# Kernel tuning notes

Hardware: AMD Instinct MI355X
Metric: run time of the kernel (lower is better)

Reference implementation:

```python
import jax, jax.numpy as jnp
import numpy as np

H = 768      # hidden_size
NH = 12      # num_heads
HD = H // NH # head_size
MLP = 3072
B, N = 16, 577


def setup_inputs() -> dict:
    key = jax.random.key(0)
    ks = jax.random.split(key, 16)
    s = 0.02
    return {
        "x": jax.random.normal(ks[0], (B, N, H), jnp.float32),
        "Wq": jax.random.normal(ks[1], (H, H), jnp.float32) * s,
        "bq": jnp.zeros((H,), jnp.float32),
        "Wk": jax.random.normal(ks[2], (H, H), jnp.float32) * s,
        "bk": jnp.zeros((H,), jnp.float32),
        "Wv": jax.random.normal(ks[3], (H, H), jnp.float32) * s,
        "bv": jnp.zeros((H,), jnp.float32),
        "Wo": jax.random.normal(ks[4], (H, H), jnp.float32) * s,
        "bo": jnp.zeros((H,), jnp.float32),
        "W1": jax.random.normal(ks[5], (H, MLP), jnp.float32) * s,
        "b1": jnp.zeros((MLP,), jnp.float32),
        "W2": jax.random.normal(ks[6], (MLP, H), jnp.float32) * s,
        "b2": jnp.zeros((H,), jnp.float32),
        "ln1_g": jnp.ones((H,), jnp.float32),
        "ln1_b": jnp.zeros((H,), jnp.float32),
        "ln2_g": jnp.ones((H,), jnp.float32),
        "ln2_b": jnp.zeros((H,), jnp.float32),
    }


def _layernorm(x, g, b, eps=1e-6):
    mu = jnp.mean(x, axis=-1, keepdims=True)
    var = jnp.mean(jnp.square(x - mu), axis=-1, keepdims=True)
    return (x - mu) * jax.lax.rsqrt(var + eps) * g + b


def reference(x, Wq, bq, Wk, bk, Wv, bv, Wo, bo, W1, b1, W2, b2,
              ln1_g, ln1_b, ln2_g, ln2_b):
    h = x
    y = _layernorm(x, ln1_g, ln1_b)
    # projections [B,N,H] -> [B,NH,N,HD]
    def heads(t):
        return t.reshape(B, N, NH, HD).transpose(0, 2, 1, 3)
    q = heads(y @ Wq + bq)
    _k = heads(y @ Wk + bk)  # computed but UNUSED (bug in original: Q@V^T)
    v = heads(y @ Wv + bv)
    # faithful to source: scores = Q @ V^T (not K)
    scores = jnp.einsum('bhqd,bhkd->bhqk', q, v) / jnp.sqrt(jnp.float32(HD))
    probs = jax.nn.softmax(scores, axis=-1)
    o = jnp.einsum('bhqk,bhkd->bhqd', probs, v)
    o = o.transpose(0, 2, 1, 3).reshape(B, N, H)
    attn_out = o @ Wo + bo
    x1 = attn_out + h
    h2 = x1
    y2 = _layernorm(x1, ln2_g, ln2_b)
    m = jax.nn.gelu(y2 @ W1 + b1, approximate=False)
    m = m @ W2 + b2
    return m + h2
```

## Files before the change

### kernel.cpp

```cpp
#include <hip/hip_runtime.h>


#define GLOBAL_AS __attribute__((address_space(1)))
#define LDS_AS __attribute__((address_space(3)))

typedef __bf16 bf16x8 __attribute__((ext_vector_type(8)));
typedef float f32x4 __attribute__((ext_vector_type(4)));
typedef unsigned short u16x8 __attribute__((ext_vector_type(8)));

static __device__ __forceinline__ f32x4 mfma16(bf16x8 a, bf16x8 b, f32x4 c) {
  return __builtin_amdgcn_mfma_f32_16x16x32_bf16(a, b, c, 0, 0, 0);
}

static __device__ __forceinline__ unsigned short f2bf(float f) {
  union { float f; unsigned u; } v; v.f = f;
  unsigned r = v.u + 0x7fffu + ((v.u >> 16) & 1u);
  return (unsigned short)(r >> 16);
}

static __device__ __forceinline__ void async16(const void* g, void* l) {
  __builtin_amdgcn_global_load_lds((const GLOBAL_AS void*)g, (LDS_AS void*)l, 16, 0, 0);
}

static __device__ __forceinline__ float gelu_exact(float x) {
  return 0.5f * x * (1.0f + erff(x * 0.70710678118654752f));
}

static __device__ __forceinline__ void tc_body(const float* __restrict__ W,
                                               unsigned short* __restrict__ Wt,
                                               int K, int ldw, int nb, int kb,
                                               int t) {
  __shared__ float tile[32][33];
  const int tr = t >> 5, tc = t & 31;
#pragma unroll
  for (int p = 0; p < 4; ++p)
    tile[p * 8 + tr][tc] = W[(size_t)(kb + p * 8 + tr) * ldw + nb + tc];
  __syncthreads();
#pragma unroll
  for (int p = 0; p < 4; ++p)
    Wt[(size_t)(nb + p * 8 + tr) * K + kb + tc] = f2bf(tile[tc][p * 8 + tr]);
}

__global__ __launch_bounds__(256)
void transpose_all(const float* __restrict__ Wq, const float* __restrict__ Wv,
                   const float* __restrict__ Wo, const float* __restrict__ W1,
                   const float* __restrict__ W2, unsigned short* __restrict__ R3) {
  const size_t S = 589824;
  int id = blockIdx.x;
  const int t = threadIdx.x;
  if (id < 1728) {
    const float* W = id < 576 ? Wq : (id < 1152 ? Wv : Wo);
    unsigned short* dst = R3 + (size_t)(id / 576) * S;
    id %= 576;
    tc_body(W, dst, 768, 768, (id % 24) * 32, (id / 24) * 32, t);
  } else {
    id -= 1728;
    const int seg = id / 1152;
    id %= 1152;
    const int s = seg >> 1;
    if ((seg & 1) == 0) {
      unsigned short* dst = R3 + 3 * S + (size_t)s * 4 * S;
      tc_body(W1 + s * 1536, dst, 768, 3072, (id % 48) * 32, (id / 48) * 32, t);
    } else {
      unsigned short* dst = R3 + 5 * S + (size_t)s * 4 * S;
      tc_body(W2 + (size_t)s * 1536 * 768, dst, 1536, 768, (id % 24) * 32,
              (id / 24) * 32, t);
    }
  }
}

__global__ __launch_bounds__(256)
void ln_f32(const float* __restrict__ x, const float* __restrict__ g,
            const float* __restrict__ be, unsigned short* __restrict__ y) {
  const int w = threadIdx.x >> 6, lane = threadIdx.x & 63;
  const size_t row = (size_t)blockIdx.x * 4 + w;
  const float* xr = x + row * 768;
  float vv[12];
#pragma unroll
  for (int j = 0; j < 3; ++j) {
    float4 v = *(const float4*)(xr + j * 256 + lane * 4);
    vv[j * 4 + 0] = v.x; vv[j * 4 + 1] = v.y;
    vv[j * 4 + 2] = v.z; vv[j * 4 + 3] = v.w;
  }
  float s = 0.f;
#pragma unroll
  for (int j = 0; j < 12; ++j) s += vv[j];
#pragma unroll
  for (int o = 32; o > 0; o >>= 1) s += __shfl_xor(s, o);
  const float mu = s * (1.0f / 768.0f);
  float q = 0.f;
#pragma unroll
  for (int j = 0; j < 12; ++j) { float d = vv[j] - mu; q += d * d; }
#pragma unroll
  for (int o = 32; o > 0; o >>= 1) q += __shfl_xor(q, o);
  const float rstd = rsqrtf(q * (1.0f / 768.0f) + 1e-6f);
  unsigned short* yr = y + row * 768;
#pragma unroll
  for (int j = 0; j < 3; ++j) {
    float4 gv = *(const float4*)(g + j * 256 + lane * 4);
    float4 bv = *(const float4*)(be + j * 256 + lane * 4);
    ushort4 o4;
    o4.x = f2bf((vv[j * 4 + 0] - mu) * rstd * gv.x + bv.x);
    o4.y = f2bf((vv[j * 4 + 1] - mu) * rstd * gv.y + bv.y);
    o4.z = f2bf((vv[j * 4 + 2] - mu) * rstd * gv.z + bv.z);
    o4.w = f2bf((vv[j * 4 + 3] - mu) * rstd * gv.w + bv.w);
    *(ushort4*)(yr + j * 256 + lane * 4) = o4;
  }
}

template <int ACT, int RES, int OUTF32, int NB, int SPLIT>
__global__ __launch_bounds__(256, 2)
void gemm_bt(const unsigned short* __restrict__ A,
             const unsigned short* __restrict__ B,
             const float* __restrict__ bias,
             const float* __restrict__ bias2,
             const float* __restrict__ resid,
             void* __restrict__ out1, void* __restrict__ out2,
             int M, int N, int K) {
  __shared__ __align__(16) unsigned short As[2][128 * 32];
  __shared__ __align__(16) unsigned short Bs[2][128 * 32];
  const int t = threadIdx.x;
  const int nwg = gridDim.x;
  const int q8 = nwg >> 3, r8 = nwg & 7;
  const int xcd = blockIdx.x & 7, jj = blockIdx.x >> 3;
  const int wgid = (xcd < r8 ? xcd * (q8 + 1) : r8 * (q8 + 1) + (xcd - r8) * q8) + jj;
  const int gn = N >> 7;
  const int m0 = (wgid / gn) * 128;
  const int n0 = (wgid % gn) * 128;
  const int w = t >> 6, lane = t & 63;
  const int lr = lane & 15, lg = lane >> 4;
  const int wrr = (w >> 1) * 64, wcc = (w & 1) * 64;
  f32x4 acc[4][4] = {};

  auto stage = [&](int buf, int k0) {
#pragma unroll
    for (int p = 0; p < 2; ++p) {
      int i = p * 256 + t;
      int row = i >> 2, c = (i & 3) << 3;
      int ar = m0 + row; ar = ar < M ? ar : M - 1;
      async16(A + (size_t)ar * K + k0 + c, &As[buf][i * 8]);
      async16(B + (size_t)(n0 + row) * K + k0 + c, &Bs[buf][i * 8]);
    }
  };

  stage(0, 0);
  int cur = 0;
  const int nt = K >> 5;
  for (int tt = 0; tt < nt; ++tt) {
    if (tt + 1 < nt) {
      stage(cur ^ 1, (tt + 1) << 5);
      asm volatile("s_waitcnt vmcnt(4)" ::: "memory");
    } else {
      asm volatile("s_waitcnt vmcnt(0)" ::: "memory");
    }
    __builtin_amdgcn_s_barrier();
    bf16x8 af[4], bfr[4];
#pragma unroll
    for (int mi = 0; mi < 4; ++mi)
      af[mi] = *(const bf16x8*)(&As[cur][(wrr + mi * 16 + lr) * 32 + lg * 8]);
#pragma unroll
    for (int ni = 0; ni < 4; ++ni)
      bfr[ni] = *(const bf16x8*)(&Bs[cur][(wcc + ni * 16 + lr) * 32 + lg * 8]);
    asm volatile("s_waitcnt lgkmcnt(0)" ::: "memory");
    __builtin_amdgcn_sched_barrier(0);
    __builtin_amdgcn_s_barrier();
#pragma unroll
    for (int mi = 0; mi < 4; ++mi)
#pragma unroll
      for (int ni = 0; ni < 4; ++ni)
        acc[mi][ni] = mfma16(af[mi], bfr[ni], acc[mi][ni]);
    cur ^= 1;
  }
  const int orow = m0 + wrr + lg * 4;
  const int ocol = n0 + wcc + lr;
#pragma unroll
  for (int mi = 0; mi < 4; ++mi) {
#pragma unroll
    for (int ni = 0; ni < 4; ++ni) {
      const int col = ocol + ni * 16;
      float bs;
      if (SPLIT)
        bs = (col < 768) ? bias[col] : bias2[col - 768];
      else
        bs = NB ? 0.f : bias[col];
      f32x4 a = acc[mi][ni];
#pragma unroll
      for (int r = 0; r < 4; ++r) {
        const int row = orow + mi * 16 + r;
        if (row < M) {
          float v = a[r] + bs;
          if (ACT == 1) v = gelu_exact(v);
          if (RES == 1) v += resid[(size_t)row * N + col];
          if (SPLIT) {
            if (col < 768)
              ((unsigned short*)out1)[(size_t)row * 768 + col] = f2bf(v);
            else
              ((unsigned short*)out2)[(size_t)row * 768 + col - 768] = f2bf(v);
          } else if (OUTF32) {
            ((float*)out1)[(size_t)row * N + col] = v;
          } else {
            ((unsigned short*)out1)[(size_t)row * N + col] = f2bf(v);
          }
        }
      }
    }
  }
}

__global__ __launch_bounds__(256, 2)
void attn_fused(const unsigned short* __restrict__ Q,
                const unsigned short* __restrict__ V,
                unsigned short* __restrict__ O) {
  __shared__ __align__(16) unsigned short Vn[64 * 72];
  __shared__ __align__(16) unsigned short Vt[64 * 72];
  __shared__ __align__(16) unsigned short Pl[4][32 * 72];
  const int qt = blockIdx.x, h = blockIdx.y, b = blockIdx.z;
  const int t = threadIdx.x, w = t >> 6, lane = t & 63;
  const int lr = lane & 15, lg = lane >> 4;
  const int q0 = qt * 128 + w * 32;
  bf16x8 aq[2][2];
#pragma unroll
  for (int mi = 0; mi < 2; ++mi) {
    int qrow = q0 + mi * 16 + lr; qrow = qrow < 577 ? qrow : 576;
    const unsigned short* qp = Q + ((size_t)(b * 577 + qrow)) * 768 + h * 64;
    aq[mi][0] = *(const bf16x8*)(qp + lg * 8);
    aq[mi][1] = *(const bf16x8*)(qp + 32 + lg * 8);
  }
  bf16x8 ones;
#pragma unroll
  for (int j = 0; j < 8; ++j) ones[j] = (__bf16)1.0f;
  f32x4 oacc[2][4] = {};
  f32x4 lac[2] = {};
  const unsigned short* vp = V + (size_t)b * 577 * 768 + h * 64;

  for (int kt = 0; kt < 10; ++kt) {
    const int k0 = kt * 64;
#pragma unroll
    for (int p = 0; p < 2; ++p) {
      int i = p * 256 + t;
      int kr = i >> 3, c = (i & 7) << 3;
      int gk = k0 + kr; gk = gk < 577 ? gk : 576;
      bf16x8 vv = *(const bf16x8*)(vp + (size_t)gk * 768 + c);
      *(bf16x8*)(Vn + kr * 72 + c) = vv;
    }
    __syncthreads();
#pragma unroll
    for (int p = 0; p < 2; ++p) {
      int i = p * 256 + t;
      int d = i & 63, kb = (i >> 6) * 8;
      u16x8 tv;
#pragma unroll
      for (int j = 0; j < 8; ++j) tv[j] = Vn[(kb + j) * 72 + d];
      *(u16x8*)(Vt + d * 72 + kb) = tv;
    }
    f32x4 s[2][4];
#pragma unroll
    for (int mi = 0; mi < 2; ++mi)
#pragma unroll
      for (int ni = 0; ni < 4; ++ni) {
        f32x4 a = {};
        a = mfma16(aq[mi][0], *(const bf16x8*)(Vn + (ni * 16 + lr) * 72 + lg * 8), a);
        a = mfma16(aq[mi][1], *(const bf16x8*)(Vn + (ni * 16 + lr) * 72 + 32 + lg * 8), a);
        s[mi][ni] = a * 0.125f;
      }
    if (kt == 9) {
#pragma unroll
      for (int ni = 0; ni < 4; ++ni) {
        int kc = k0 + ni * 16 + lr;
        if (kc >= 577) {
#pragma unroll
          for (int mi = 0; mi < 2; ++mi) {
            s[mi][ni][0] = -1e30f; s[mi][ni][1] = -1e30f;
            s[mi][ni][2] = -1e30f; s[mi][ni][3] = -1e30f;
          }
        }
      }
    }
#pragma unroll
    for (int mi = 0; mi < 2; ++mi)
#pragma unroll
      for (int ni = 0; ni < 4; ++ni)
#pragma unroll
        for (int r = 0; r < 4; ++r)
          Pl[w][(mi * 16 + lg * 4 + r) * 72 + ni * 16 + lr] =
              f2bf(__expf(s[mi][ni][r]));
    __syncthreads();
#pragma unroll
    for (int mi = 0; mi < 2; ++mi) {
      const bf16x8 pa0 = *(const bf16x8*)(&Pl[w][(mi * 16 + lr) * 72 + lg * 8]);
      const bf16x8 pa1 = *(const bf16x8*)(&Pl[w][(mi * 16 + lr) * 72 + 32 + lg * 8]);
#pragma unroll
      for (int di = 0; di < 4; ++di) {
        oacc[mi][di] = mfma16(pa0, *(const bf16x8*)(Vt + (di * 16 + lr) * 72 + lg * 8), oacc[mi][di]);
        oacc[mi][di] = mfma16(pa1, *(const bf16x8*)(Vt + (di * 16 + lr) * 72 + 32 + lg * 8), oacc[mi][di]);
      }
      lac[mi] = mfma16(pa0, ones, lac[mi]);
      lac[mi] = mfma16(pa1, ones, lac[mi]);
    }
  }
#pragma unroll
  for (int mi = 0; mi < 2; ++mi)
#pragma unroll
    for (int r = 0; r < 4; ++r) {
      const int qg = q0 + mi * 16 + lg * 4 + r;
      if (qg < 577) {
        const float inv = 1.0f / lac[mi][r];
        unsigned short* op = O + ((size_t)(b * 577 + qg)) * 768 + h * 64 + lr;
#pragma unroll
        for (int di = 0; di < 4; ++di) op[di * 16] = f2bf(oacc[mi][di][r] * inv);
      }
    }
}

extern "C" void kernel_launch(void* const* d_in, const int* in_sizes, int n_in,
                              void* d_out, int out_size, void* d_ws, size_t ws_size,
                              hipStream_t stream) {
  (void)in_sizes; (void)n_in; (void)out_size; (void)ws_size;
  const float* x   = (const float*)d_in[0];
  const float* Wq  = (const float*)d_in[1];
  const float* bq  = (const float*)d_in[2];
  const float* Wv  = (const float*)d_in[5];
  const float* bv  = (const float*)d_in[6];
  const float* Wo  = (const float*)d_in[7];
  const float* bo  = (const float*)d_in[8];
  const float* W1  = (const float*)d_in[9];
  const float* b1  = (const float*)d_in[10];
  const float* W2  = (const float*)d_in[11];
  const float* b2  = (const float*)d_in[12];
  const float* g1  = (const float*)d_in[13];
  const float* be1 = (const float*)d_in[14];
  const float* g2  = (const float*)d_in[15];
  const float* be2 = (const float*)d_in[16];
  float* out = (float*)d_out;

  const size_t BF = (size_t)9232 * 768 * 2;
  const size_t S = 589824;
  char* ws = (char*)d_ws;
  unsigned short* R0 = (unsigned short*)(ws);
  unsigned short* R1 = (unsigned short*)(ws + BF);
  unsigned short* R2 = (unsigned short*)(ws + 2 * BF);
  unsigned short* R3 = (unsigned short*)(ws + 3 * BF);
  unsigned short* WqT = R3;
  unsigned short* WoT = R3 + 2 * S;
  unsigned short* W1T0 = R3 + 3 * S;
  unsigned short* W2T0 = R3 + 5 * S;
  unsigned short* W1T1 = R3 + 7 * S;
  unsigned short* W2T1 = R3 + 9 * S;
  unsigned short* mb = R1;

  dim3 blk(256);

  transpose_all<<<dim3(6336), blk, 0, stream>>>(Wq, Wv, Wo, W1, W2, R3);

  ln_f32<<<dim3(2308), blk, 0, stream>>>(x, g1, be1, R0);

  gemm_bt<0, 0, 0, 0, 1><<<dim3(876), blk, 0, stream>>>(
      R0, WqT, bq, bv, nullptr, R1, R2, 9232, 1536, 768);

  attn_fused<<<dim3(5, 12, 16), blk, 0, stream>>>(R1, R2, R0);

  gemm_bt<0, 1, 1, 0, 0><<<dim3(438), blk, 0, stream>>>(
      R0, WoT, bo, nullptr, x, out, nullptr, 9232, 768, 768);

  ln_f32<<<dim3(2308), blk, 0, stream>>>(out, g2, be2, R0);

  gemm_bt<1, 0, 0, 0, 0><<<dim3(876), blk, 0, stream>>>(
      R0, W1T0, b1, nullptr, nullptr, mb, nullptr, 9232, 1536, 768);
  gemm_bt<0, 1, 1, 0, 0><<<dim3(438), blk, 0, stream>>>(
      mb, W2T0, b2, nullptr, out, out, nullptr, 9232, 768, 1536);
  gemm_bt<1, 0, 0, 0, 0><<<dim3(876), blk, 0, stream>>>(
      R0, W1T1, b1 + 1536, nullptr, nullptr, mb, nullptr, 9232, 1536, 768);
  gemm_bt<0, 1, 1, 1, 0><<<dim3(438), blk, 0, stream>>>(
      mb, W2T1, nullptr, nullptr, out, out, nullptr, 9232, 768, 1536);
}
```

Measured before the change: 341.9 us.

## Give each wave private LDS tiles to eliminate block-wide barriers in GEMM

Restructures the GEMM so each of the four waves stages its own 64-row A and B slices into private LDS buffers, removing both s_barrier calls per k-step. The wait count is adjusted for the larger number of outstanding async loads per thread. This removes cross-wave synchronisation stalls. In exchange, A and B tiles are no longer shared between waves, which doubles global/L2 load traffic and LDS footprint per block.

```diff
diff --git a/kernel.cpp b/kernel.cpp
--- a/kernel.cpp
+++ b/kernel.cpp
@@ -110,15 +110,15 @@
 
 template <int ACT, int RES, int OUTF32, int NB, int SPLIT>
 __global__ __launch_bounds__(256, 2)
-void gemm_bt(const unsigned short* __restrict__ A,
+void gemm_wp(const unsigned short* __restrict__ A,
              const unsigned short* __restrict__ B,
              const float* __restrict__ bias,
              const float* __restrict__ bias2,
              const float* __restrict__ resid,
              void* __restrict__ out1, void* __restrict__ out2,
              int M, int N, int K) {
-  __shared__ __align__(16) unsigned short As[2][128 * 32];
-  __shared__ __align__(16) unsigned short Bs[2][128 * 32];
+  __shared__ __align__(16) unsigned short LA[4][2][64 * 32];
+  __shared__ __align__(16) unsigned short LB[4][2][64 * 32];
   const int t = threadIdx.x;
   const int nwg = gridDim.x;
   const int q8 = nwg >> 3, r8 = nwg & 7;
@@ -134,12 +134,17 @@
 
   auto stage = [&](int buf, int k0) {
 #pragma unroll
-    for (int p = 0; p < 2; ++p) {
-      int i = p * 256 + t;
-      int row = i >> 2, c = (i & 3) << 3;
-      int ar = m0 + row; ar = ar < M ? ar : M - 1;
-      async16(A + (size_t)ar * K + k0 + c, &As[buf][i * 8]);
-      async16(B + (size_t)(n0 + row) * K + k0 + c, &Bs[buf][i * 8]);
+    for (int p = 0; p < 4; ++p) {
+      int ch = p * 64 + lane;
+      int row = ch >> 2, cc = (ch & 3) << 3;
+      int ar = m0 + wrr + row; ar = ar < M ? ar : M - 1;
+      async16(A + (size_t)ar * K + k0 + cc, &LA[w][buf][ch * 8]);
+    }
+#pragma unroll
+    for (int p = 0; p < 4; ++p) {
+      int ch = p * 64 + lane;
+      int row = ch >> 2, cc = (ch & 3) << 3;
+      async16(B + (size_t)(n0 + wcc + row) * K + k0 + cc, &LB[w][buf][ch * 8]);
     }
   };
 
@@ -149,21 +154,19 @@
   for (int tt = 0; tt < nt; ++tt) {
     if (tt + 1 < nt) {
       stage(cur ^ 1, (tt + 1) << 5);
-      asm volatile("s_waitcnt vmcnt(4)" ::: "memory");
+      asm volatile("s_waitcnt vmcnt(8)" ::: "memory");
     } else {
       asm volatile("s_waitcnt vmcnt(0)" ::: "memory");
     }
-    __builtin_amdgcn_s_barrier();
     bf16x8 af[4], bfr[4];
 #pragma unroll
     for (int mi = 0; mi < 4; ++mi)
-      af[mi] = *(const bf16x8*)(&As[cur][(wrr + mi * 16 + lr) * 32 + lg * 8]);
+      af[mi] = *(const bf16x8*)(&LA[w][cur][(mi * 16 + lr) * 32 + lg * 8]);
 #pragma unroll
     for (int ni = 0; ni < 4; ++ni)
-      bfr[ni] = *(const bf16x8*)(&Bs[cur][(wcc + ni * 16 + lr) * 32 + lg * 8]);
+      bfr[ni] = *(const bf16x8*)(&LB[w][cur][(ni * 16 + lr) * 32 + lg * 8]);
     asm volatile("s_waitcnt lgkmcnt(0)" ::: "memory");
     __builtin_amdgcn_sched_barrier(0);
-    __builtin_amdgcn_s_barrier();
 #pragma unroll
     for (int mi = 0; mi < 4; ++mi)
 #pragma unroll
@@ -354,22 +357,22 @@
 
   ln_f32<<<dim3(2308), blk, 0, stream>>>(x, g1, be1, R0);
 
-  gemm_bt<0, 0, 0, 0, 1><<<dim3(876), blk, 0, stream>>>(
+  gemm_wp<0, 0, 0, 0, 1><<<dim3(876), blk, 0, stream>>>(
       R0, WqT, bq, bv, nullptr, R1, R2, 9232, 1536, 768);
 
   attn_fused<<<dim3(5, 12, 16), blk, 0, stream>>>(R1, R2, R0);
 
-  gemm_bt<0, 1, 1, 0, 0><<<dim3(438), blk, 0, stream>>>(
+  gemm_wp<0, 1, 1, 0, 0><<<dim3(438), blk, 0, stream>>>(
       R0, WoT, bo, nullptr, x, out, nullptr, 9232, 768, 768);
 
   ln_f32<<<dim3(2308), blk, 0, stream>>>(out, g2, be2, R0);
 
-  gemm_bt<1, 0, 0, 0, 0><<<dim3(876), blk, 0, stream>>>(
+  gemm_wp<1, 0, 0, 0, 0><<<dim3(876), blk, 0, stream>>>(
       R0, W1T0, b1, nullptr, nullptr, mb, nullptr, 9232, 1536, 768);
-  gemm_bt<0, 1, 1, 0, 0><<<dim3(438), blk, 0, stream>>>(
+  gemm_wp<0, 1, 1, 0, 0><<<dim3(438), blk, 0, stream>>>(
       mb, W2T0, b2, nullptr, out, out, nullptr, 9232, 768, 1536);
-  gemm_bt<1, 0, 0, 0, 0><<<dim3(876), blk, 0, stream>>>(
+  gemm_wp<1, 0, 0, 0, 0><<<dim3(876), blk, 0, stream>>>(
       R0, W1T1, b1 + 1536, nullptr, nullptr, mb, nullptr, 9232, 1536, 768);
-  gemm_bt<0, 1, 1, 1, 0><<<dim3(438), blk, 0, stream>>>(
+  gemm_wp<0, 1, 1, 1, 0><<<dim3(438), blk, 0, stream>>>(
       mb, W2T1, nullptr, nullptr, out, out, nullptr, 9232, 768, 1536);
 }
```

Result: slower. 421.1 us (+23.2%).
